# Kernel optimization log

Measured on AMD Instinct MI355X. Metric: run time of the kernel, lower is better.

The kernel has to match this reference:

```python
import jax, jax.numpy as jnp
import numpy as np

BN_EPS = 1e-5

def _l2norm(x, axis):
    # F.normalize: x / max(||x||_2, 1e-12)
    n = jnp.sqrt(jnp.sum(x * x, axis=axis, keepdims=True))
    return x / jnp.maximum(n, 1e-12)

def _psi(x_bhc, w, g, b):
    # 1x1 conv over HW-as-channels: [B,HW,C] x [D,HW] -> [B,D,C]
    y = jnp.einsum('dh,bhc->bdc', w, x_bhc)
    # inference BatchNorm2d with running_mean=0, running_var=1
    scale = g / jnp.sqrt(1.0 + BN_EPS)
    y = y * scale[None, :, None] + b[None, :, None]
    return jax.nn.relu(y)

def setup_inputs() -> dict:
    key = jax.random.key(0)
    ks = jax.random.split(key, 8)
    B, C, H, W, D = 16, 2048, 32, 32, 256
    return {
        'v2l_conv_feature': jax.random.normal(ks[0], (B, C, H, W), jnp.float32),
        'l2v_conv_feature': jax.random.normal(ks[1], (B, C, H, W), jnp.float32),
        'w_v2l': jax.random.normal(ks[2], (D, H * W), jnp.float32) * 0.02,
        'g_v2l': jax.random.uniform(ks[3], (D,), jnp.float32, 0.5, 1.5),
        'b_v2l': jax.random.normal(ks[4], (D,), jnp.float32) * 0.1,
        'w_l2v': jax.random.normal(ks[5], (D, H * W), jnp.float32) * 0.02,
        'g_l2v': jax.random.uniform(ks[6], (D,), jnp.float32, 0.5, 1.5),
        'b_l2v': jax.random.normal(ks[7], (D,), jnp.float32) * 0.1,
    }

def reference(v2l_conv_feature, l2v_conv_feature, w_v2l, g_v2l, b_v2l, w_l2v, g_l2v, b_l2v):
    B, C, H, W = v2l_conv_feature.shape
    HW = H * W
    xv = jnp.transpose(v2l_conv_feature.reshape(B, C, HW), (0, 2, 1))  # [B,HW,C]
    xl = jnp.transpose(l2v_conv_feature.reshape(B, C, HW), (0, 2, 1))  # [B,HW,C]
    v2l_adj = _l2norm(_psi(xv, w_v2l, g_v2l, b_v2l), axis=2)  # [B,D,C], norm over C
    l2v_adj = _l2norm(_psi(xl, w_l2v, g_l2v, b_l2v), axis=1)  # [B,D,C], norm over D
    # Faithful to torch: reshape of the permuted tensor is a raw row-major
    # reinterpretation [B,HW,C] -> [B,C,HW] (NOT a transpose back).
    xv_r = xv.reshape(B, C, HW)
    latent = jnp.einsum('bdc,bch->bdh', v2l_adj, xv_r)          # [B,D,HW]
    latent_n = _l2norm(latent, axis=-1)
    aff = jax.nn.softmax(jnp.einsum('bdh,beh->bde', latent_n, latent_n), axis=-1)  # [B,D,D]
    latent = jnp.einsum('bde,beh->bdh', aff, latent)            # [B,D,HW]
    visible = jnp.einsum('bdc,bdh->bch', l2v_adj, latent)       # [B,C,HW]
    return visible.reshape(B, C, H, W)
```

## Files before the change

### kernel.cpp

```cpp
#include <hip/hip_runtime.h>
#include <hip/hip_bf16.h>

#define BB 16
#define CC 2048
#define HWW 1024
#define DD 256
#define BN_RSQRT 0.9999950000374997f

typedef short bf16x8 __attribute__((ext_vector_type(8)));
typedef float f32x4 __attribute__((ext_vector_type(4)));
typedef unsigned short u16x8 __attribute__((ext_vector_type(8)));
typedef unsigned short u16x4 __attribute__((ext_vector_type(4)));
typedef unsigned short u16;

typedef __attribute__((address_space(1))) const unsigned GU;
typedef __attribute__((address_space(3))) unsigned LU;
__device__ __forceinline__ void gload16(const void* g, void* l) {
    __builtin_amdgcn_global_load_lds((GU*)g, (LU*)l, 16, 0, 0);
}

__device__ __forceinline__ unsigned short f2bf(float x) {
    unsigned u = __builtin_bit_cast(unsigned, x);
    unsigned r = u + 0x7FFFu + ((u >> 16) & 1u);
    return (unsigned short)(r >> 16);
}
__device__ __forceinline__ float bf2f(unsigned short h) {
    unsigned u = ((unsigned)h) << 16;
    return __builtin_bit_cast(float, u);
}
__device__ __forceinline__ void split2(float x, unsigned short& hi, unsigned short& lo) {
    hi = f2bf(x);
    lo = f2bf(x - bf2f(hi));
}
__device__ __forceinline__ void split2t(float x, unsigned short& hi, unsigned short& lo) {
    hi = f2bf(x);
    float d = x - bf2f(hi);
    lo = (unsigned short)(__builtin_bit_cast(unsigned, d) >> 16);
}

struct RegsA { u16x8 h[2]; u16x8 l[2]; };
struct RegsB { u16x8 h[2]; u16x8 l[2]; };

__global__ __launch_bounds__(256) void split_k(const float* __restrict__ in,
                                               u16* __restrict__ hi, u16* __restrict__ lo,
                                               long long n8) {
    long long i = (long long)blockIdx.x * 256 + threadIdx.x;
    if (i >= n8) return;
    const float4* p = (const float4*)in + i * 2;
    float4 a = p[0], b = p[1];
    float xs[8] = {a.x, a.y, a.z, a.w, b.x, b.y, b.z, b.w};
    u16x8 h, l;
    #pragma unroll
    for (int j = 0; j < 8; ++j) { unsigned short hh, ll; split2(xs[j], hh, ll); h[j] = hh; l[j] = ll; }
    *(u16x8*)(hi + i * 8) = h;
    *(u16x8*)(lo + i * 8) = l;
}

template <int BF, int EPI, int FUSE2, int KS>
__global__ __launch_bounds__(512, 2) void gemm8(
    const u16* __restrict__ Ah0, const u16* __restrict__ Al0,
    const u16* __restrict__ Ah1, const u16* __restrict__ Al1,
    long long aB, int lda,
    const void* __restrict__ B0a, const void* __restrict__ B0b,
    const void* __restrict__ B1a, const void* __restrict__ B1b,
    long long bB, int ldb,
    float* __restrict__ C0, float* __restrict__ C1,
    long long cB, long long kB, int ldc,
    int K,
    const float* __restrict__ g0, const float* __restrict__ bb0,
    const float* __restrict__ g1, const float* __restrict__ bb1)
{
    __shared__ __attribute__((aligned(16))) char smem[2][65536];

    const int gx = gridDim.x, gy = gridDim.y;
    int nwg = gx * gy * gridDim.z;
    int id = blockIdx.x + gx * (blockIdx.y + gy * blockIdx.z);
    int chunk = nwg >> 3;
    int nid = (id & 7) * chunk + (id >> 3);
    int bx = nid % gx;
    int tmp = nid / gx;
    int by = tmp % gy;
    int bz = tmp / gy;

    const int t = threadIdx.x;
    const int n0 = bx * 256, m0 = by * 256;

    int op = 0, batch, kz = 0;
    if constexpr (FUSE2) { op = bz >> 4; batch = bz & 15; }
    else if constexpr (KS > 1) { batch = bz / KS; kz = bz - batch * KS; }
    else { batch = bz; }
    const int koffA = kz * K;

    const u16* Ahp = (op ? Ah1 : Ah0) + (long long)batch * aB + koffA;
    const u16* Alp = (op ? Al1 : Al0) + (long long)batch * aB + koffA;
    const float* Bf = nullptr;
    const u16* Bh = nullptr;
    const u16* Bl = nullptr;
    if constexpr (BF == 0) {
        Bf = (const float*)(op ? B1a : B0a) + (long long)batch * bB;
        Bf += ((long long)(koffA >> 10)) * 1024 * ldb + (koffA & 1023);
    } else {
        Bh = (const u16*)(op ? B1a : B0a) + (long long)batch * bB;
        Bl = (const u16*)(op ? B1b : B0b) + (long long)batch * bB;
    }
    float* Cb = ((EPI == 1 && FUSE2) ? (op ? C1 : C0) : C0)
              + (long long)batch * cB + (long long)kz * kB;
    const float* gp = op ? g1 : g0;
    const float* bp = op ? bb1 : bb0;

    const int arow = t >> 2;
    const int aslt = (t & 3) ^ ((t >> 3) & 3);
    const int brow = t >> 3;
    const int bslt = (t & 7) ^ ((t >> 3) & 7);

    const int l = t & 63, w = t >> 6;
    const int wr = w >> 2, wc = w & 3;
    const int rl = l & 15, kq = l >> 4;
    const int fsw = (kq ^ ((rl >> 1) & 3)) * 16;

    f32x4 acc[8][4];
    #pragma unroll
    for (int i = 0; i < 8; ++i)
        #pragma unroll
        for (int j = 0; j < 4; ++j)
            acc[i][j] = (f32x4){0.f, 0.f, 0.f, 0.f};

    auto gstage = [&](int k0, char* sn) {
        const u16* pa = Ahp + (long long)(m0 + arow) * lda + k0 + aslt * 8;
        gload16(pa,                        sn + t * 16);
        gload16(pa + (long long)128 * lda, sn + 8192 + t * 16);
        const u16* pl = Alp + (long long)(m0 + arow) * lda + k0 + aslt * 8;
        gload16(pl,                        sn + 16384 + t * 16);
        gload16(pl + (long long)128 * lda, sn + 24576 + t * 16);
        if constexpr (BF == 0) {
            const float* pb = Bf + (long long)(n0 + brow) * ldb + k0 + bslt * 4;
            #pragma unroll
            for (int kk = 0; kk < 4; ++kk)
                gload16(pb + (long long)(64 * kk) * ldb,
                        sn + 32768 + kk * 8192 + t * 16);
        } else {
            const u16* pbh = Bh + (long long)(n0 + arow) * ldb + k0 + aslt * 8;
            gload16(pbh,                        sn + 32768 + t * 16);
            gload16(pbh + (long long)128 * ldb, sn + 40960 + t * 16);
            const u16* pbl = Bl + (long long)(n0 + arow) * ldb + k0 + aslt * 8;
            gload16(pbl,                        sn + 49152 + t * 16);
            gload16(pbl + (long long)128 * ldb, sn + 57344 + t * 16);
        }
    };

    auto readA = [&](const char* sb, int q, bf16x8* fah, bf16x8* fal) {
        #pragma unroll
        for (int i2 = 0; i2 < 4; ++i2) {
            int row = wr * 128 + (q * 4 + i2) * 16 + rl;
            int off = row * 64 + fsw;
            fah[i2] = *(const bf16x8*)(sb + off);
            fal[i2] = *(const bf16x8*)(sb + 16384 + off);
        }
    };
    auto readB = [&](const char* sb, bf16x8* fbh, bf16x8* fbl) {
        #pragma unroll
        for (int j = 0; j < 4; ++j) {
            int row = wc * 64 + j * 16 + rl;
            if constexpr (BF == 0) {
                const char* p = sb + 32768 + row * 128;
                int g = rl & 7;
                float4 x0 = *(const float4*)(p + ((2 * kq) ^ g) * 16);
                float4 x1 = *(const float4*)(p + ((2 * kq + 1) ^ g) * 16);
                float xs[8] = {x0.x, x0.y, x0.z, x0.w, x1.x, x1.y, x1.z, x1.w};
                u16x8 h, lo;
                #pragma unroll
                for (int e = 0; e < 8; ++e) {
                    unsigned short hh, ll; split2t(xs[e], hh, ll);
                    h[e] = hh; lo[e] = ll;
                }
                fbh[j] = __builtin_bit_cast(bf16x8, h);
                fbl[j] = __builtin_bit_cast(bf16x8, lo);
            } else {
                int off = row * 64 + fsw;
                fbh[j] = *(const bf16x8*)(sb + 32768 + off);
                fbl[j] = *(const bf16x8*)(sb + 49152 + off);
            }
        }
    };

    const int NIT = K >> 5;

    gstage(0, smem[0]);
    asm volatile("s_waitcnt vmcnt(0)" ::: "memory");
    __builtin_amdgcn_s_barrier();

    for (int it = 0; it < NIT; ++it) {
        char* sb = smem[it & 1];
        char* sn = smem[(it + 1) & 1];
        if (it + 1 < NIT) gstage((it + 1) << 5, sn);

        bf16x8 fbh[4], fbl[4], fah[4], fal[4];
        readB(sb, fbh, fbl);
        readA(sb, 0, fah, fal);
        __builtin_amdgcn_s_barrier();

        __builtin_amdgcn_s_setprio(1);
        #pragma unroll
        for (int i2 = 0; i2 < 4; ++i2)
            #pragma unroll
            for (int j = 0; j < 4; ++j)
                acc[i2][j] = __builtin_amdgcn_mfma_f32_16x16x32_bf16(fal[i2], fbh[j], acc[i2][j], 0, 0, 0);
        #pragma unroll
        for (int i2 = 0; i2 < 4; ++i2)
            #pragma unroll
            for (int j = 0; j < 4; ++j)
                acc[i2][j] = __builtin_amdgcn_mfma_f32_16x16x32_bf16(fah[i2], fbl[j], acc[i2][j], 0, 0, 0);
        #pragma unroll
        for (int i2 = 0; i2 < 4; ++i2)
            #pragma unroll
            for (int j = 0; j < 4; ++j)
                acc[i2][j] = __builtin_amdgcn_mfma_f32_16x16x32_bf16(fah[i2], fbh[j], acc[i2][j], 0, 0, 0);
        __builtin_amdgcn_s_setprio(0);
        __builtin_amdgcn_s_barrier();

        readA(sb, 1, fah, fal);
        __builtin_amdgcn_s_setprio(1);
        #pragma unroll
        for (int i2 = 0; i2 < 4; ++i2)
            #pragma unroll
            for (int j = 0; j < 4; ++j)
                acc[4 + i2][j] = __builtin_amdgcn_mfma_f32_16x16x32_bf16(fal[i2], fbh[j], acc[4 + i2][j], 0, 0, 0);
        #pragma unroll
        for (int i2 = 0; i2 < 4; ++i2)
            #pragma unroll
            for (int j = 0; j < 4; ++j)
                acc[4 + i2][j] = __builtin_amdgcn_mfma_f32_16x16x32_bf16(fah[i2], fbl[j], acc[4 + i2][j], 0, 0, 0);
        #pragma unroll
        for (int i2 = 0; i2 < 4; ++i2)
            #pragma unroll
            for (int j = 0; j < 4; ++j)
                acc[4 + i2][j] = __builtin_amdgcn_mfma_f32_16x16x32_bf16(fah[i2], fbh[j], acc[4 + i2][j], 0, 0, 0);
        __builtin_amdgcn_s_setprio(0);
        asm volatile("s_waitcnt vmcnt(0)" ::: "memory");
        __builtin_amdgcn_s_barrier();
    }

    #pragma unroll
    for (int i = 0; i < 8; ++i) {
        #pragma unroll
        for (int r = 0; r < 4; ++r) {
            int row = m0 + wr * 128 + i * 16 + kq * 4 + r;
            float sc = 1.0f, bi = 0.0f;
            if (EPI == 1) { sc = gp[row] * BN_RSQRT; bi = bp[row]; }
            #pragma unroll
            for (int j = 0; j < 4; ++j) {
                int col = n0 + wc * 64 + j * 16 + rl;
                float v = acc[i][j][r];
                if (EPI == 1) v = fmaxf(fmaf(v, sc, bi), 0.0f);
                Cb[(long long)row * ldc + col] = v;
            }
        }
    }
}

template <int BN_, int EPI>
__global__ __launch_bounds__(256) void mfma_gemm(
    const void* __restrict__ Ap, const void* __restrict__ Ap2, long long aB, int lda,
    const void* __restrict__ Bp, const void* __restrict__ Bp2, long long bB, int ldb,
    void* __restrict__ Cp, void* __restrict__ Cp2,
    long long cB, int ldc, int K)
{
    constexpr int NJ   = BN_ / 32;
    constexpr int BNB  = BN_ * 64;
    constexpr int BUFB = 16384 + BN_ * 128;
    __shared__ __attribute__((aligned(16))) char smem[2][BUFB];

    const int gx = gridDim.x, gy = gridDim.y;
    int nwg = gx * gy * gridDim.z;
    int id = blockIdx.x + gx * (blockIdx.y + gy * blockIdx.z);
    int chunk = nwg >> 3;
    int nid = (id & 7) * chunk + (id >> 3);
    int bx = nid % gx;
    int tmp = nid / gx;
    int by = tmp % gy;
    int bz = tmp / gy;

    const int t  = threadIdx.x;
    const int n0 = bx * BN_;
    const int m0 = by * 128;

    const int ar = t >> 1, ag = t & 1;
    const int af = (ar >> 1) & 3;
    const int as0 = (2 * ag) ^ af, as1 = (2 * ag + 1) ^ af;
    const bool bact = (BN_ == 128) || (t < 2 * BN_);
    const int br = (t >> 1) & (BN_ - 1), bg = t & 1;
    const int bf = (br >> 1) & 3;
    const int bs0 = (2 * bg) ^ bf, bs1 = (2 * bg + 1) ^ bf;

    const int l  = t & 63, w = t >> 6;
    const int wr = w >> 1, wc = w & 1;
    const int rl = l & 15, kq = l >> 4;
    const int sw = kq ^ ((rl >> 1) & 3);
    const int aoff = (wr * 64 + rl) * 64 + sw * 16;
    const int boff = (wc * (BN_ / 2) + rl) * 64 + sw * 16;

    const u16* Ahp = (const u16*)Ap  + (long long)bz * aB;
    const u16* Alp = (const u16*)Ap2 + (long long)bz * aB;
    const u16* Bhp = (const u16*)Bp  + (long long)bz * bB;
    const u16* Blp = (const u16*)Bp2 + (long long)bz * bB;

    auto loadA = [&](int k0, RegsA& ra) {
        const u16* ph = Ahp + (long long)(m0 + ar) * lda + k0 + ag * 16;
        const u16* pl = Alp + (long long)(m0 + ar) * lda + k0 + ag * 16;
        ra.h[0] = *(const u16x8*)(ph);
        ra.h[1] = *(const u16x8*)(ph + 8);
        ra.l[0] = *(const u16x8*)(pl);
        ra.l[1] = *(const u16x8*)(pl + 8);
    };
    auto loadB = [&](int k0, RegsB& rb) {
        if (!bact) return;
        const u16* ph = Bhp + (long long)(n0 + br) * ldb + k0 + bg * 16;
        const u16* pl = Blp + (long long)(n0 + br) * ldb + k0 + bg * 16;
        rb.h[0] = *(const u16x8*)(ph);
        rb.h[1] = *(const u16x8*)(ph + 8);
        rb.l[0] = *(const u16x8*)(pl);
        rb.l[1] = *(const u16x8*)(pl + 8);
    };
    auto stageWrite = [&](char* sb, RegsA& ra, RegsB& rb) {
        *(u16x8*)(sb + ar * 64 + as0 * 16) = ra.h[0];
        *(u16x8*)(sb + ar * 64 + as1 * 16) = ra.h[1];
        *(u16x8*)(sb + 8192 + ar * 64 + as0 * 16) = ra.l[0];
        *(u16x8*)(sb + 8192 + ar * 64 + as1 * 16) = ra.l[1];
        if (bact) {
            char* sB = sb + 16384;
            *(u16x8*)(sB + br * 64 + bs0 * 16) = rb.h[0];
            *(u16x8*)(sB + br * 64 + bs1 * 16) = rb.h[1];
            *(u16x8*)(sB + BNB + br * 64 + bs0 * 16) = rb.l[0];
            *(u16x8*)(sB + BNB + br * 64 + bs1 * 16) = rb.l[1];
        }
    };

    f32x4 acc[4][NJ];
    #pragma unroll
    for (int i = 0; i < 4; ++i)
        #pragma unroll
        for (int j = 0; j < NJ; ++j)
            acc[i][j] = (f32x4){0.f, 0.f, 0.f, 0.f};

    RegsA a0, a1;
    RegsB b0, b1;
    const int NIT = K >> 5;

    loadA(0, a0); loadB(0, b0);
    stageWrite(smem[0], a0, b0);
    loadA(32, a1); loadB(32, b1);
    asm volatile("s_waitcnt lgkmcnt(0)" ::: "memory");
    __builtin_amdgcn_s_barrier();

    auto step = [&](int it, char* sb, char* sn, RegsA& pa, RegsB& pb,
                    RegsA& qa, RegsB& qb) {
        bf16x8 fah[4], fal[4], fbh[NJ], fbl[NJ];
        #pragma unroll
        for (int i = 0; i < 4; ++i) {
            fah[i] = *(const bf16x8*)(sb + aoff + i * 1024);
            fal[i] = *(const bf16x8*)(sb + 8192 + aoff + i * 1024);
        }
        #pragma unroll
        for (int j = 0; j < NJ; ++j) {
            fbh[j] = *(const bf16x8*)(sb + 16384 + boff + j * 1024);
            fbl[j] = *(const bf16x8*)(sb + 16384 + BNB + boff + j * 1024);
        }
        if (it + 1 < NIT) stageWrite(sn, pa, pb);
        if (it + 2 < NIT) { loadA((it + 2) << 5, qa); loadB((it + 2) << 5, qb); }
        #pragma unroll
        for (int i = 0; i < 4; ++i)
            #pragma unroll
            for (int j = 0; j < NJ; ++j) {
                acc[i][j] = __builtin_amdgcn_mfma_f32_16x16x32_bf16(fal[i], fbh[j], acc[i][j], 0, 0, 0);
                acc[i][j] = __builtin_amdgcn_mfma_f32_16x16x32_bf16(fah[i], fbl[j], acc[i][j], 0, 0, 0);
                acc[i][j] = __builtin_amdgcn_mfma_f32_16x16x32_bf16(fah[i], fbh[j], acc[i][j], 0, 0, 0);
            }
        asm volatile("s_waitcnt lgkmcnt(0)" ::: "memory");
        __builtin_amdgcn_s_barrier();
    };

    for (int it = 0; it < NIT; it += 2) {
        step(it,     smem[0], smem[1], a1, b1, a0, b0);
        step(it + 1, smem[1], smem[0], a0, b0, a1, b1);
    }

    #pragma unroll
    for (int i = 0; i < 4; ++i) {
        #pragma unroll
        for (int r = 0; r < 4; ++r) {
            int row = m0 + wr * 64 + i * 16 + kq * 4 + r;
            #pragma unroll
            for (int j = 0; j < NJ; ++j) {
                int col = n0 + wc * (BN_ / 2) + j * 16 + rl;
                float v = acc[i][j][r];
                if constexpr (EPI == 0) {
                    ((float*)Cp + (long long)bz * cB)[(long long)row * ldc + col] = v;
                } else {
                    unsigned short hh, ll; split2(v, hh, ll);
                    ((u16*)Cp  + (long long)bz * cB)[(long long)row * ldc + col] = hh;
                    ((u16*)Cp2 + (long long)bz * cB)[(long long)row * ldc + col] = ll;
                }
            }
        }
    }
}

__global__ __launch_bounds__(256) void rownorm_split_perm_k(float* __restrict__ Y) {
    int d = blockIdx.x, b = blockIdx.y, t = threadIdx.x;
    float* row = Y + ((long long)b * DD + d) * CC;
    float4 v0 = ((const float4*)row)[2 * t];
    float4 v1 = ((const float4*)row)[2 * t + 1];
    float s = v0.x * v0.x + v0.y * v0.y + v0.z * v0.z + v0.w * v0.w
            + v1.x * v1.x + v1.y * v1.y + v1.z * v1.z + v1.w * v1.w;
    for (int off = 32; off > 0; off >>= 1) s += __shfl_down(s, off, 64);
    __shared__ float wsum[4];
    __shared__ float ivs;
    int lane = t & 63, w = t >> 6;
    if (lane == 0) wsum[w] = s;
    __syncthreads();
    if (t == 0) ivs = 1.0f / fmaxf(sqrtf(wsum[0] + wsum[1] + wsum[2] + wsum[3]), 1e-12f);
    __syncthreads();
    float iv = ivs;
    float xs[8] = {v0.x * iv, v0.y * iv, v0.z * iv, v0.w * iv,
                   v1.x * iv, v1.y * iv, v1.z * iv, v1.w * iv};
    u16x4 he, ho, le, lo4;
    #pragma unroll
    for (int j = 0; j < 4; ++j) {
        unsigned short hh, ll;
        split2(xs[2 * j], hh, ll);       he[j] = hh; le[j] = ll;
        split2(xs[2 * j + 1], hh, ll);   ho[j] = hh; lo4[j] = ll;
    }
    u16* hi = (u16*)row;
    *(u16x4*)(hi + 4 * t) = he;
    *(u16x4*)(hi + 1024 + 4 * t) = ho;
    *(u16x4*)(hi + 2048 + 4 * t) = le;
    *(u16x4*)(hi + 3072 + 4 * t) = lo4;
}

__global__ __launch_bounds__(256) void colnorm_k(const float* __restrict__ Yl,
                                                 float* __restrict__ rsc) {
    int b = blockIdx.y;
    int c = blockIdx.x * 256 + threadIdx.x;
    const float* base = Yl + (long long)b * DD * CC + c;
    float s = 0.0f;
    for (int d = 0; d < DD; ++d) { float v = base[(long long)d * CC]; s += v * v; }
    rsc[(long long)b * CC + c] = 1.0f / fmaxf(sqrtf(s), 1e-12f);
}

__global__ __launch_bounds__(256) void trans_split_k(const float* __restrict__ in,
                                                     const float* __restrict__ scale,
                                                     u16* __restrict__ hi, u16* __restrict__ lo) {
    __shared__ float tile[32][33];
    int s0 = blockIdx.x * 32, r0 = blockIdx.y * 32, b = blockIdx.z;
    const float* inb = in + (long long)b * DD * CC;
    int tx = threadIdx.x & 31, ty = threadIdx.x >> 5;
    for (int i = ty; i < 32; i += 8)
        tile[i][tx] = inb[(long long)(r0 + i) * CC + s0 + tx];
    __syncthreads();
    for (int i = ty; i < 32; i += 8) {
        float v = tile[tx][i] * scale[(long long)b * CC + s0 + i];
        unsigned short hh, ll; split2(v, hh, ll);
        long long o = (long long)b * DD * CC + (long long)(s0 + i) * DD + r0 + tx;
        hi[o] = hh; lo[o] = ll;
    }
}

__global__ __launch_bounds__(256) void latreduce_k(const float* __restrict__ parts,
                                                   u16* __restrict__ hi, u16* __restrict__ lo,
                                                   u16* __restrict__ thi, u16* __restrict__ tlo) {
    __shared__ float tile[32][33];
    int h0 = blockIdx.x * 32, d0 = blockIdx.y * 32, b = blockIdx.z;
    const long long sL = (long long)DD * HWW;
    const long long ps = (long long)BB * sL;
    const float* base = parts + (long long)b * sL;
    int tx = threadIdx.x & 31, ty = threadIdx.x >> 5;
    for (int i = ty; i < 32; i += 8) {
        long long o = (long long)(d0 + i) * HWW + h0 + tx;
        float s = base[o] + base[o + ps] + base[o + 2 * ps] + base[o + 3 * ps];
        tile[i][tx] = s;
        unsigned short hh, ll; split2(s, hh, ll);
        long long od = (long long)b * sL + o;
        hi[od] = hh; lo[od] = ll;
    }
    __syncthreads();
    for (int i = ty; i < 32; i += 8) {
        float v = tile[tx][i];
        unsigned short hh, ll; split2(v, hh, ll);
        long long ot = (long long)b * sL + (long long)(h0 + i) * DD + d0 + tx;
        thi[ot] = hh; tlo[ot] = ll;
    }
}

__global__ __launch_bounds__(256) void latnorm_k(const float* __restrict__ G,
                                                 float* __restrict__ rs) {
    int i = blockIdx.x * 256 + threadIdx.x;
    int b = i >> 8, d = i & 255;
    float v = G[((long long)b * DD + d) * DD + d];
    rs[i] = 1.0f / fmaxf(sqrtf(v), 1e-12f);
}

__global__ __launch_bounds__(256) void softmax_k(const float* __restrict__ G,
                                                 const float* __restrict__ rs,
                                                 u16* __restrict__ affHi,
                                                 u16* __restrict__ affLo) {
    int d = blockIdx.x, b = blockIdx.y;
    const float* row = G + ((long long)b * DD + d) * DD;
    const float* rsb = rs + (long long)b * DD;
    int t = threadIdx.x;
    float lg = row[t] * rsb[d] * rsb[t];

    float m = lg;
    for (int off = 32; off > 0; off >>= 1) m = fmaxf(m, __shfl_down(m, off, 64));
    __shared__ float wsm[4];
    __shared__ float bm, bs;
    int lane = t & 63, w = t >> 6;
    if (lane == 0) wsm[w] = m;
    __syncthreads();
    if (t == 0) bm = fmaxf(fmaxf(wsm[0], wsm[1]), fmaxf(wsm[2], wsm[3]));
    __syncthreads();
    float e = expf(lg - bm);
    float s = e;
    for (int off = 32; off > 0; off >>= 1) s += __shfl_down(s, off, 64);
    if (lane == 0) wsm[w] = s;
    __syncthreads();
    if (t == 0) bs = wsm[0] + wsm[1] + wsm[2] + wsm[3];
    __syncthreads();
    float v = e / bs;
    unsigned short hh, ll; split2(v, hh, ll);
    long long o = ((long long)b * DD + d) * DD + t;
    affHi[o] = hh; affLo[o] = ll;
}

extern "C" void kernel_launch(void* const* d_in, const int* in_sizes, int n_in,
                              void* d_out, int out_size, void* d_ws, size_t ws_size,
                              hipStream_t stream) {
    const float* v2l   = (const float*)d_in[0];
    const float* l2v   = (const float*)d_in[1];
    const float* w_v2l = (const float*)d_in[2];
    const float* g_v2l = (const float*)d_in[3];
    const float* b_v2l = (const float*)d_in[4];
    const float* w_l2v = (const float*)d_in[5];
    const float* g_l2v = (const float*)d_in[6];
    const float* b_l2v = (const float*)d_in[7];
    float* out = (float*)d_out;

    char* W = (char*)d_ws;
    float* Yv     = (float*)(W + 0);
    float* Yl     = (float*)(W + 33554432);
    u16*   YltHi  = (u16*)(W + 67108864);
    u16*   YltLo  = (u16*)(W + 83886080);
    u16*   latHi  = (u16*)(W + 100663296);
    u16*   latLo  = (u16*)(W + 109051904);
    u16*   latTHi = (u16*)(W + 117440512);
    u16*   latTLo = (u16*)(W + 125829120);
    u16*   l2tHi  = (u16*)(W + 134217728);
    u16*   l2tLo  = (u16*)(W + 142606336);
    float* gram   = (float*)(W + 150994944);
    float* rs     = (float*)(W + 155189248);
    float* rsc    = (float*)(W + 155205632);
    u16*   affHi  = (u16*)(W + 155336704);
    u16*   affLo  = (u16*)(W + 157433856);
    u16*   WvHi   = (u16*)(W + 159531008);
    u16*   WvLo   = WvHi + 262144;
    u16*   WlHi   = WvLo + 262144;
    u16*   WlLo   = WlHi + 262144;

    float* latPart = (float*)d_out;

    const long long sY   = (long long)DD * CC;
    const long long sL   = (long long)DD * HWW;
    const long long sG   = (long long)DD * DD;
    const long long sX   = (long long)CC * HWW;
    const long long sYp  = (long long)DD * 4096;

    split_k<<<128, 256, 0, stream>>>(w_v2l, WvHi, WvLo, 32768);
    split_k<<<128, 256, 0, stream>>>(w_l2v, WlHi, WlLo, 32768);

    gemm8<0, 1, 1, 1><<<dim3(CC / 256, 1, 32), 512, 0, stream>>>(
        WvHi, WvLo, WlHi, WlLo, 0, HWW,
        v2l, nullptr, l2v, nullptr, sX, HWW,
        Yv, Yl, sY, 0, CC, HWW,
        g_v2l, b_v2l, g_l2v, b_l2v);

    rownorm_split_perm_k<<<dim3(DD, BB), 256, 0, stream>>>(Yv);
    colnorm_k<<<dim3(CC / 256, BB), 256, 0, stream>>>(Yl, rsc);
    trans_split_k<<<dim3(CC / 32, DD / 32, BB), 256, 0, stream>>>(Yl, rsc, YltHi, YltLo);

    gemm8<0, 0, 0, 4><<<dim3(HWW / 256, 1, 64), 512, 0, stream>>>(
        (const u16*)Yv, (const u16*)Yv + 2048, nullptr, nullptr, sYp, 4096,
        v2l, nullptr, nullptr, nullptr, sX, HWW,
        latPart, nullptr, sL, (long long)BB * sL, HWW, 512,
        nullptr, nullptr, nullptr, nullptr);

    latreduce_k<<<dim3(HWW / 32, DD / 32, BB), 256, 0, stream>>>(
        latPart, latHi, latLo, latTHi, latTLo);

    mfma_gemm<64, 0><<<dim3(4, 2, BB), 256, 0, stream>>>(
        latHi, latLo, sL, HWW, latHi, latLo, sL, HWW,
        gram, nullptr, sG, DD, HWW);

    latnorm_k<<<dim3(BB * DD / 256), 256, 0, stream>>>(gram, rs);
    softmax_k<<<dim3(DD, BB), 256, 0, stream>>>(gram, rs, affHi, affLo);

    mfma_gemm<128, 2><<<dim3(2, 8, BB), 256, 0, stream>>>(
        latTHi, latTLo, sL, DD, affHi, affLo, sG, DD,
        l2tHi, l2tLo, sL, DD, DD);

    gemm8<1, 0, 0, 1><<<dim3(HWW / 256, CC / 256, BB), 512, 0, stream>>>(
        YltHi, YltLo, nullptr, nullptr, sY, DD,
        l2tHi, l2tLo, nullptr, nullptr, sL, DD,
        out, nullptr, sX, 0, HWW, DD,
        nullptr, nullptr, nullptr, nullptr);
}
```

Baseline: 380.8 us.

## Shrink GEMM tiles to 128x128, raise occupancy, halve split-K for latent GEMM

Replaces the 256x256 split-bf16 GEMM kernel with a 128x128-tile variant that uses half the LDS and allows four workgroups per CU. Each K step now runs a single MFMA phase with one barrier instead of two half-phases. The latent GEMM drops from split-K 4 to split-K 2, and the reduction kernel sums two partials instead of four. This trades lower per-tile reuse and extra global traffic for more parallelism and latency hiding.

```diff
diff --git a/kernel.cpp b/kernel.cpp
--- a/kernel.cpp
+++ b/kernel.cpp
@@ -57,7 +57,7 @@
 }
 
 template <int BF, int EPI, int FUSE2, int KS>
-__global__ __launch_bounds__(512, 2) void gemm8(
+__global__ __launch_bounds__(512, 4) void gemm2b(
     const u16* __restrict__ Ah0, const u16* __restrict__ Al0,
     const u16* __restrict__ Ah1, const u16* __restrict__ Al1,
     long long aB, int lda,
@@ -70,7 +70,7 @@
     const float* __restrict__ g0, const float* __restrict__ bb0,
     const float* __restrict__ g1, const float* __restrict__ bb1)
 {
-    __shared__ __attribute__((aligned(16))) char smem[2][65536];
+    __shared__ __attribute__((aligned(16))) char smem[2][32768];
 
     const int gx = gridDim.x, gy = gridDim.y;
     int nwg = gx * gy * gridDim.z;
@@ -83,7 +83,7 @@
     int bz = tmp / gy;
 
     const int t = threadIdx.x;
-    const int n0 = bx * 256, m0 = by * 256;
+    const int n0 = bx * 128, m0 = by * 128;
 
     int op = 0, batch, kz = 0;
     if constexpr (FUSE2) { op = bz >> 4; batch = bz & 15; }
@@ -118,51 +118,44 @@
     const int rl = l & 15, kq = l >> 4;
     const int fsw = (kq ^ ((rl >> 1) & 3)) * 16;
 
-    f32x4 acc[8][4];
+    f32x4 acc[4][2];
     #pragma unroll
-    for (int i = 0; i < 8; ++i)
-        #pragma unroll
-        for (int j = 0; j < 4; ++j)
+    for (int i = 0; i < 4; ++i)
+        #pragma unroll
+        for (int j = 0; j < 2; ++j)
             acc[i][j] = (f32x4){0.f, 0.f, 0.f, 0.f};
 
     auto gstage = [&](int k0, char* sn) {
         const u16* pa = Ahp + (long long)(m0 + arow) * lda + k0 + aslt * 8;
-        gload16(pa,                        sn + t * 16);
-        gload16(pa + (long long)128 * lda, sn + 8192 + t * 16);
+        gload16(pa, sn + t * 16);
         const u16* pl = Alp + (long long)(m0 + arow) * lda + k0 + aslt * 8;
-        gload16(pl,                        sn + 16384 + t * 16);
-        gload16(pl + (long long)128 * lda, sn + 24576 + t * 16);
+        gload16(pl, sn + 8192 + t * 16);
         if constexpr (BF == 0) {
             const float* pb = Bf + (long long)(n0 + brow) * ldb + k0 + bslt * 4;
-            #pragma unroll
-            for (int kk = 0; kk < 4; ++kk)
-                gload16(pb + (long long)(64 * kk) * ldb,
-                        sn + 32768 + kk * 8192 + t * 16);
+            gload16(pb,                       sn + 16384 + t * 16);
+            gload16(pb + (long long)64 * ldb, sn + 24576 + t * 16);
         } else {
             const u16* pbh = Bh + (long long)(n0 + arow) * ldb + k0 + aslt * 8;
-            gload16(pbh,                        sn + 32768 + t * 16);
-            gload16(pbh + (long long)128 * ldb, sn + 40960 + t * 16);
+            gload16(pbh, sn + 16384 + t * 16);
             const u16* pbl = Bl + (long long)(n0 + arow) * ldb + k0 + aslt * 8;
-            gload16(pbl,                        sn + 49152 + t * 16);
-            gload16(pbl + (long long)128 * ldb, sn + 57344 + t * 16);
-        }
-    };
-
-    auto readA = [&](const char* sb, int q, bf16x8* fah, bf16x8* fal) {
+            gload16(pbl, sn + 24576 + t * 16);
+        }
+    };
+
+    auto readA = [&](const char* sb, bf16x8* fah, bf16x8* fal) {
         #pragma unroll
         for (int i2 = 0; i2 < 4; ++i2) {
-            int row = wr * 128 + (q * 4 + i2) * 16 + rl;
-            int off = row * 64 + fsw;
+            int off = (wr * 64 + i2 * 16 + rl) * 64 + fsw;
             fah[i2] = *(const bf16x8*)(sb + off);
-            fal[i2] = *(const bf16x8*)(sb + 16384 + off);
+            fal[i2] = *(const bf16x8*)(sb + 8192 + off);
         }
     };
     auto readB = [&](const char* sb, bf16x8* fbh, bf16x8* fbl) {
         #pragma unroll
-        for (int j = 0; j < 4; ++j) {
-            int row = wc * 64 + j * 16 + rl;
+        for (int j = 0; j < 2; ++j) {
+            int row = wc * 32 + j * 16 + rl;
             if constexpr (BF == 0) {
-                const char* p = sb + 32768 + row * 128;
+                const char* p = sb + 16384 + row * 128;
                 int g = rl & 7;
                 float4 x0 = *(const float4*)(p + ((2 * kq) ^ g) * 16);
                 float4 x1 = *(const float4*)(p + ((2 * kq + 1) ^ g) * 16);
@@ -177,8 +170,8 @@
                 fbl[j] = __builtin_bit_cast(bf16x8, lo);
             } else {
                 int off = row * 64 + fsw;
-                fbh[j] = *(const bf16x8*)(sb + 32768 + off);
-                fbl[j] = *(const bf16x8*)(sb + 49152 + off);
+                fbh[j] = *(const bf16x8*)(sb + 16384 + off);
+                fbl[j] = *(const bf16x8*)(sb + 24576 + off);
             }
         }
     };
@@ -192,64 +185,45 @@
     for (int it = 0; it < NIT; ++it) {
         char* sb = smem[it & 1];
         char* sn = smem[(it + 1) & 1];
-        if (it + 1 < NIT) gstage((it + 1) << 5, sn);
-
-        bf16x8 fbh[4], fbl[4], fah[4], fal[4];
+        const bool more = (it + 1) < NIT;
+        if (more) gstage((it + 1) << 5, sn);
+
+        bf16x8 fah[4], fal[4], fbh[2], fbl[2];
         readB(sb, fbh, fbl);
-        readA(sb, 0, fah, fal);
-        __builtin_amdgcn_s_barrier();
+        readA(sb, fah, fal);
 
         __builtin_amdgcn_s_setprio(1);
         #pragma unroll
         for (int i2 = 0; i2 < 4; ++i2)
             #pragma unroll
-            for (int j = 0; j < 4; ++j)
+            for (int j = 0; j < 2; ++j)
                 acc[i2][j] = __builtin_amdgcn_mfma_f32_16x16x32_bf16(fal[i2], fbh[j], acc[i2][j], 0, 0, 0);
         #pragma unroll
         for (int i2 = 0; i2 < 4; ++i2)
             #pragma unroll
-            for (int j = 0; j < 4; ++j)
+            for (int j = 0; j < 2; ++j)
                 acc[i2][j] = __builtin_amdgcn_mfma_f32_16x16x32_bf16(fah[i2], fbl[j], acc[i2][j], 0, 0, 0);
         #pragma unroll
         for (int i2 = 0; i2 < 4; ++i2)
             #pragma unroll
-            for (int j = 0; j < 4; ++j)
+            for (int j = 0; j < 2; ++j)
                 acc[i2][j] = __builtin_amdgcn_mfma_f32_16x16x32_bf16(fah[i2], fbh[j], acc[i2][j], 0, 0, 0);
         __builtin_amdgcn_s_setprio(0);
+
+        if (more) { asm volatile("s_waitcnt vmcnt(0)" ::: "memory"); }
         __builtin_amdgcn_s_barrier();
-
-        readA(sb, 1, fah, fal);
-        __builtin_amdgcn_s_setprio(1);
-        #pragma unroll
-        for (int i2 = 0; i2 < 4; ++i2)
-            #pragma unroll
-            for (int j = 0; j < 4; ++j)
-                acc[4 + i2][j] = __builtin_amdgcn_mfma_f32_16x16x32_bf16(fal[i2], fbh[j], acc[4 + i2][j], 0, 0, 0);
-        #pragma unroll
-        for (int i2 = 0; i2 < 4; ++i2)
-            #pragma unroll
-            for (int j = 0; j < 4; ++j)
-                acc[4 + i2][j] = __builtin_amdgcn_mfma_f32_16x16x32_bf16(fah[i2], fbl[j], acc[4 + i2][j], 0, 0, 0);
-        #pragma unroll
-        for (int i2 = 0; i2 < 4; ++i2)
-            #pragma unroll
-            for (int j = 0; j < 4; ++j)
-                acc[4 + i2][j] = __builtin_amdgcn_mfma_f32_16x16x32_bf16(fah[i2], fbh[j], acc[4 + i2][j], 0, 0, 0);
-        __builtin_amdgcn_s_setprio(0);
-        asm volatile("s_waitcnt vmcnt(0)" ::: "memory");
-        __builtin_amdgcn_s_barrier();
     }
 
     #pragma unroll
-    for (int i = 0; i < 8; ++i) {
+    for (int i = 0; i < 4; ++i) {
         #pragma unroll
         for (int r = 0; r < 4; ++r) {
-            int row = m0 + wr * 128 + i * 16 + kq * 4 + r;
+            int row = m0 + wr * 64 + i * 16 + kq * 4 + r;
             float sc = 1.0f, bi = 0.0f;
             if (EPI == 1) { sc = gp[row] * BN_RSQRT; bi = bp[row]; }
             #pragma unroll
-            for (int j = 0; j < 4; ++j) {
-                int col = n0 + wc * 64 + j * 16 + rl;
+            for (int j = 0; j < 2; ++j) {
+                int col = n0 + wc * 32 + j * 16 + rl;
                 float v = acc[i][j][r];
                 if (EPI == 1) v = fmaxf(fmaf(v, sc, bi), 0.0f);
                 Cb[(long long)row * ldc + col] = v;
@@ -476,7 +450,7 @@
     int tx = threadIdx.x & 31, ty = threadIdx.x >> 5;
     for (int i = ty; i < 32; i += 8) {
         long long o = (long long)(d0 + i) * HWW + h0 + tx;
-        float s = base[o] + base[o + ps] + base[o + 2 * ps] + base[o + 3 * ps];
+        float s = base[o] + base[o + ps];
         tile[i][tx] = s;
         unsigned short hh, ll; split2(s, hh, ll);
         long long od = (long long)b * sL + o;
@@ -576,7 +550,7 @@
     split_k<<<128, 256, 0, stream>>>(w_v2l, WvHi, WvLo, 32768);
     split_k<<<128, 256, 0, stream>>>(w_l2v, WlHi, WlLo, 32768);
 
-    gemm8<0, 1, 1, 1><<<dim3(CC / 256, 1, 32), 512, 0, stream>>>(
+    gemm2b<0, 1, 1, 1><<<dim3(CC / 128, DD / 128, 32), 512, 0, stream>>>(
         WvHi, WvLo, WlHi, WlLo, 0, HWW,
         v2l, nullptr, l2v, nullptr, sX, HWW,
         Yv, Yl, sY, 0, CC, HWW,
@@ -586,10 +560,10 @@
     colnorm_k<<<dim3(CC / 256, BB), 256, 0, stream>>>(Yl, rsc);
     trans_split_k<<<dim3(CC / 32, DD / 32, BB), 256, 0, stream>>>(Yl, rsc, YltHi, YltLo);
 
-    gemm8<0, 0, 0, 4><<<dim3(HWW / 256, 1, 64), 512, 0, stream>>>(
+    gemm2b<0, 0, 0, 2><<<dim3(HWW / 128, DD / 128, 32), 512, 0, stream>>>(
         (const u16*)Yv, (const u16*)Yv + 2048, nullptr, nullptr, sYp, 4096,
         v2l, nullptr, nullptr, nullptr, sX, HWW,
-        latPart, nullptr, sL, (long long)BB * sL, HWW, 512,
+        latPart, nullptr, sL, (long long)BB * sL, HWW, 1024,
         nullptr, nullptr, nullptr, nullptr);
 
     latreduce_k<<<dim3(HWW / 32, DD / 32, BB), 256, 0, stream>>>(
@@ -606,7 +580,7 @@
         latTHi, latTLo, sL, DD, affHi, affLo, sG, DD,
         l2tHi, l2tLo, sL, DD, DD);
 
-    gemm8<1, 0, 0, 1><<<dim3(HWW / 256, CC / 256, BB), 512, 0, stream>>>(
+    gemm2b<1, 0, 0, 1><<<dim3(HWW / 128, CC / 128, BB), 512, 0, stream>>>(
         YltHi, YltLo, nullptr, nullptr, sY, DD,
         l2tHi, l2tLo, nullptr, nullptr, sL, DD,
         out, nullptr, sX, 0, HWW, DD,
```

After: 364.8 us. 4.2% less time.
